# Kernel optimization log

Measured on AMD Instinct MI355X. Metric: run time of the kernel, lower is better.

Reference implementation:

```python
import jax, jax.numpy as jnp
import numpy as np

NUM_HEADS = 8
LN_EPS = 1e-5


def _layernorm(x, g, b):
    m = jnp.mean(x, axis=-1, keepdims=True)
    v = jnp.mean(jnp.square(x - m), axis=-1, keepdims=True)
    return (x - m) * jax.lax.rsqrt(v + LN_EPS) * g + b


def setup_inputs() -> dict:
    key = jax.random.key(0)
    ks = jax.random.split(key, 10)
    D, C, Cin = 2, 256, 64  # depth, embed dim, input channels
    w = lambda k, shape: jax.random.normal(k, shape, jnp.float32) * 0.02
    return {
        "x": jax.random.normal(ks[0], (4, Cin, 12, 12, 12), jnp.float32),
        "W_pe": w(ks[1], (Cin, C)),
        "b_pe": jnp.zeros((C,), jnp.float32),
        "cls_token": w(ks[2], (1, 1, C)),
        "ln1_g": jnp.ones((D, C), jnp.float32),
        "ln1_b": jnp.zeros((D, C), jnp.float32),
        "Wqkv": w(ks[3], (D, C, 3 * C)),
        "Wproj": w(ks[4], (D, C, C)),
        "bproj": jnp.zeros((D, C), jnp.float32),
        "ln2_g": jnp.ones((D, C), jnp.float32),
        "ln2_b": jnp.zeros((D, C), jnp.float32),
        "W1": w(ks[5], (D, C, C)),
        "b1": jnp.zeros((D, C), jnp.float32),
        "W2": w(ks[6], (D, C, C)),
        "b2": jnp.zeros((D, C), jnp.float32),
        "normf_g": jnp.ones((C,), jnp.float32),
        "normf_b": jnp.zeros((C,), jnp.float32),
    }


def reference(x, W_pe, b_pe, cls_token, ln1_g, ln1_b, Wqkv, Wproj, bproj,
              ln2_g, ln2_b, W1, b1, W2, b2, normf_g, normf_b):
    B, Cin, H, W, L = x.shape
    C = W_pe.shape[1]
    hd = C // NUM_HEADS
    scale = hd ** (-0.5)

    # PatchEmbed: 1x1x1 Conv3d == per-voxel linear projection, then flatten to tokens
    tok = jnp.einsum('bchwl,cd->bhwld', x, W_pe).reshape(B, H * W * L, C) + b_pe
    cls = jnp.broadcast_to(cls_token, (B, 1, C))
    t = jnp.concatenate([cls, tok], axis=1)  # [B, N, C], N = H*W*L + 1
    N = t.shape[1]

    depth = Wqkv.shape[0]
    for i in range(depth):
        # --- self-attention ---
        y = _layernorm(t, ln1_g[i], ln1_b[i])
        qkv = (y @ Wqkv[i]).reshape(B, N, 3, NUM_HEADS, hd)
        qkv = jnp.transpose(qkv, (2, 0, 3, 1, 4))  # [3, B, H, N, hd]
        q, k, v = qkv[0], qkv[1], qkv[2]
        attn = jnp.einsum('bhnd,bhmd->bhnm', q, k) * scale
        attn = jax.nn.softmax(attn, axis=-1)
        o = jnp.einsum('bhnm,bhmd->bhnd', attn, v)
        o = jnp.transpose(o, (0, 2, 1, 3)).reshape(B, N, C)
        t = t + (o @ Wproj[i] + bproj[i])
        # --- MLP (mlp_ratio=1.0, exact GELU) ---
        y = _layernorm(t, ln2_g[i], ln2_b[i])
        h = jax.nn.gelu(y @ W1[i] + b1[i], approximate=False)
        t = t + (h @ W2[i] + b2[i])

    t = _layernorm(t, normf_g, normf_b)
    x_cls = t[:, 0]                                   # [B, C]
    feat = t[:, 1:]                                   # [B, H*W*L, C]
    feat = jnp.transpose(feat, (0, 2, 1)).reshape(B, C, H, W, L)  # downsample = Identity for dim=256
    return x_cls, feat
```

## Files before the change

kernel.cpp:

```cpp
#include <hip/hip_runtime.h>
#include <hip/hip_bf16.h>
#include <math.h>

#define B_   4
#define CIN  64
#define P_   1728
#define N_   1729
#define C_   256
#define NH_  8
#define HD_  32
#define M_   (B_*N_)
#define NPAD 1792

typedef __bf16 bf16x8 __attribute__((ext_vector_type(8)));
typedef __bf16 bf16x4 __attribute__((ext_vector_type(4)));
typedef float  f32x4  __attribute__((ext_vector_type(4)));
typedef float  f32x16 __attribute__((ext_vector_type(16)));

__global__ __launch_bounds__(256) void embed2(
    const float* __restrict__ x, const float* __restrict__ Wpe,
    const float* __restrict__ bpe, const float* __restrict__ cls,
    float* __restrict__ t)
{
    int idx = blockIdx.x*256 + threadIdx.x;
    int c   = idx & 255;
    int n   = (idx >> 8) % N_;
    int b   = idx / (N_*256);
    if (n == 0) { t[idx] = cls[c]; return; }
    int p = n - 1;
    float acc = bpe[c];
    for (int ci = 0; ci < CIN; ++ci)
        acc += x[(size_t)(b*CIN + ci)*P_ + p] * Wpe[ci*C_ + c];
    t[idx] = acc;
}

__global__ __launch_bounds__(256) void ln4(
    const float* __restrict__ in, __bf16* __restrict__ out,
    const float* __restrict__ g, const float* __restrict__ bb)
{
    int wv = threadIdx.x >> 6, lane = threadIdx.x & 63;
    size_t row = (size_t)blockIdx.x*4 + wv;
    float4 v = *(const float4*)&in[row*C_ + lane*4];
    float s1 = (v.x+v.y)+(v.z+v.w);
    float s2 = (v.x*v.x+v.y*v.y)+(v.z*v.z+v.w*v.w);
    #pragma unroll
    for (int off = 32; off >= 1; off >>= 1) {
        s1 += __shfl_xor(s1, off);
        s2 += __shfl_xor(s2, off);
    }
    float mean = s1*(1.0f/C_);
    float var  = fmaxf(s2*(1.0f/C_) - mean*mean, 0.0f);
    float rstd = rsqrtf(var + 1e-5f);
    float4 gg = *(const float4*)&g[lane*4];
    float4 bv = *(const float4*)&bb[lane*4];
    bf16x4 r;
    r[0] = (__bf16)((v.x-mean)*rstd*gg.x + bv.x);
    r[1] = (__bf16)((v.y-mean)*rstd*gg.y + bv.y);
    r[2] = (__bf16)((v.z-mean)*rstd*gg.z + bv.z);
    r[3] = (__bf16)((v.w-mean)*rstd*gg.w + bv.w);
    *(bf16x4*)&out[row*C_ + lane*4] = r;
}

__global__ __launch_bounds__(256) void ln4f(
    const float* __restrict__ in, float* __restrict__ out,
    const float* __restrict__ g, const float* __restrict__ bb,
    float* __restrict__ cls_out)
{
    int wv = threadIdx.x >> 6, lane = threadIdx.x & 63;
    size_t row = (size_t)blockIdx.x*4 + wv;
    float4 v = *(const float4*)&in[row*C_ + lane*4];
    float s1 = (v.x+v.y)+(v.z+v.w);
    float s2 = (v.x*v.x+v.y*v.y)+(v.z*v.z+v.w*v.w);
    #pragma unroll
    for (int off = 32; off >= 1; off >>= 1) {
        s1 += __shfl_xor(s1, off);
        s2 += __shfl_xor(s2, off);
    }
    float mean = s1*(1.0f/C_);
    float var  = fmaxf(s2*(1.0f/C_) - mean*mean, 0.0f);
    float rstd = rsqrtf(var + 1e-5f);
    float4 gg = *(const float4*)&g[lane*4];
    float4 bv = *(const float4*)&bb[lane*4];
    float4 r;
    r.x = (v.x-mean)*rstd*gg.x + bv.x;
    r.y = (v.y-mean)*rstd*gg.y + bv.y;
    r.z = (v.z-mean)*rstd*gg.z + bv.z;
    r.w = (v.w-mean)*rstd*gg.w + bv.w;
    *(float4*)&out[row*C_ + lane*4] = r;
    if ((row % N_) == 0)
        *(float4*)&cls_out[(row / N_)*C_ + lane*4] = r;
}

__global__ __launch_bounds__(256) void wprep2(
    const float* __restrict__ Wqkv, const float* __restrict__ Wproj,
    const float* __restrict__ W1,   const float* __restrict__ W2,
    __bf16* __restrict__ wT)
{
    int z = blockIdx.z, which = z >> 1, layer = z & 1;
    const float* src; __bf16* dst; int NC;
    if (which == 0) {
        src = Wqkv + (size_t)layer*C_*768;
        dst = wT   + (size_t)layer*768*256;
        NC  = 768;
    } else {
        NC = 256;
        const float* b3 = (which == 1) ? Wproj : (which == 2) ? W1 : W2;
        src = b3 + (size_t)layer*65536;
        dst = wT + 2*768*256 + (size_t)((which-1)*2 + layer)*65536;
    }
    int n0 = blockIdx.x*32; if (n0 >= NC) return;
    int k0 = blockIdx.y*32;
    __shared__ float tile[32][33];
    int c = threadIdx.x & 31, r = threadIdx.x >> 5;
    for (int rr = r; rr < 32; rr += 8)
        tile[rr][c] = src[(size_t)(k0+rr)*NC + n0 + c];
    __syncthreads();
    for (int rr = r; rr < 32; rr += 8)
        dst[(size_t)(n0+rr)*256 + k0 + c] = (__bf16)tile[c][rr];
}

__global__ __launch_bounds__(256) void padzero(
    __bf16* __restrict__ kB, __bf16* __restrict__ vB)
{
    int idx = blockIdx.x*256 + threadIdx.x;
    if (idx >= 32*63*32) return;
    int d  = idx & 31;
    int n  = (idx >> 5) % 63 + N_;
    int bh = idx / (63*32);
    kB[((size_t)bh*NPAD + n)*32 + d] = (__bf16)0.f;
    vB[((size_t)bh*32 + d)*NPAD + n] = (__bf16)0.f;
}

template<int NC, bool ADD, bool GELU, bool BIAS, bool OUTBF>
__global__ __launch_bounds__(256) void gemm4(
    const __bf16* __restrict__ A, const __bf16* __restrict__ Wt,
    const float* __restrict__ bias, float* __restrict__ outF,
    __bf16* __restrict__ outB)
{
    __shared__ __align__(16) __bf16 As[2][64*64];
    __shared__ __align__(16) __bf16 Bs[2][64*64];
    int r0 = blockIdx.x*64, c0 = blockIdx.y*64;
    int tid = threadIdx.x;
    int wv = tid >> 6, lane = tid & 63, quad = lane >> 4, mn = lane & 15;
    int sr = tid >> 2, sc = tid & 3;
    int ga = r0 + sr; if (ga >= M_) ga = M_ - 1;

    f32x4 acc[4];
    #pragma unroll
    for (int ct = 0; ct < 4; ++ct)
        #pragma unroll
        for (int rr = 0; rr < 4; ++rr) acc[ct][rr] = 0.f;

    bf16x8 ra0, ra1, rb0, rb1;
#define GLOAD(KC) do {                                                   \
        ra0 = *(const bf16x8*)&A[(size_t)ga*256 + (KC)*64 + sc*8];       \
        ra1 = *(const bf16x8*)&A[(size_t)ga*256 + (KC)*64 + sc*8 + 32];  \
        rb0 = *(const bf16x8*)&Wt[(size_t)(c0+sr)*256 + (KC)*64 + sc*8]; \
        rb1 = *(const bf16x8*)&Wt[(size_t)(c0+sr)*256 + (KC)*64 + sc*8 + 32]; \
    } while (0)
#define SSTORE(BUF) do {                                                 \
        *(bf16x8*)&As[BUF][sr*64 + ((sc ^ (sr & 7))*8)]       = ra0;     \
        *(bf16x8*)&As[BUF][sr*64 + (((sc+4) ^ (sr & 7))*8)]   = ra1;     \
        *(bf16x8*)&Bs[BUF][sr*64 + ((sc ^ (sr & 7))*8)]       = rb0;     \
        *(bf16x8*)&Bs[BUF][sr*64 + (((sc+4) ^ (sr & 7))*8)]   = rb1;     \
    } while (0)

    GLOAD(0);
    SSTORE(0);
    __syncthreads();

    for (int kc = 0; kc < 4; ++kc) {
        int cur = kc & 1;
        if (kc < 3) GLOAD(kc+1);
        __builtin_amdgcn_sched_barrier(0);

        #pragma unroll
        for (int h = 0; h < 2; ++h) {
            bf16x8 a = *(const bf16x8*)&As[cur][(wv*16 + mn)*64 + (((h*4+quad) ^ (mn & 7))*8)];
            #pragma unroll
            for (int ct = 0; ct < 4; ++ct) {
                bf16x8 b = *(const bf16x8*)&Bs[cur][(ct*16 + mn)*64 + (((h*4+quad) ^ (mn & 7))*8)];
                acc[ct] = __builtin_amdgcn_mfma_f32_16x16x32_bf16(a, b, acc[ct], 0, 0, 0);
            }
        }

        if (kc < 3) {
            SSTORE(cur^1);
            __syncthreads();
        }
    }
#undef GLOAD
#undef SSTORE

    #pragma unroll
    for (int ct = 0; ct < 4; ++ct) {
        int col = c0 + ct*16 + mn;
        #pragma unroll
        for (int rr = 0; rr < 4; ++rr) {
            int row = r0 + wv*16 + quad*4 + rr;
            if (row >= M_) continue;
            float val = acc[ct][rr];
            if (BIAS) val += bias[col];
            if (GELU) val = 0.5f*val*(1.f + erff(val*0.70710678118654752f));
            size_t oi = (size_t)row*NC + col;
            if (OUTBF) outB[oi] = (__bf16)val;
            else if (ADD) outF[oi] += val;
            else outF[oi] = val;
        }
    }
}

__global__ __launch_bounds__(256) void gemm_qkv4(
    const __bf16* __restrict__ A, const __bf16* __restrict__ Wt,
    __bf16* __restrict__ qB, __bf16* __restrict__ kB, __bf16* __restrict__ vB)
{
    __shared__ __align__(16) __bf16 As[2][64*64];
    __shared__ __align__(16) __bf16 Bs[2][64*64];
    int r0 = blockIdx.x*64, c0 = blockIdx.y*64;
    int tid = threadIdx.x;
    int wv = tid >> 6, lane = tid & 63, quad = lane >> 4, mn = lane & 15;
    int sr = tid >> 2, sc = tid & 3;
    int ga = r0 + sr; if (ga >= M_) ga = M_ - 1;

    f32x4 acc[4];
    #pragma unroll
    for (int ct = 0; ct < 4; ++ct)
        #pragma unroll
        for (int rr = 0; rr < 4; ++rr) acc[ct][rr] = 0.f;

    bf16x8 ra0, ra1, rb0, rb1;
#define GLOAD(KC) do {                                                   \
        ra0 = *(const bf16x8*)&A[(size_t)ga*256 + (KC)*64 + sc*8];       \
        ra1 = *(const bf16x8*)&A[(size_t)ga*256 + (KC)*64 + sc*8 + 32];  \
        rb0 = *(const bf16x8*)&Wt[(size_t)(c0+sr)*256 + (KC)*64 + sc*8]; \
        rb1 = *(const bf16x8*)&Wt[(size_t)(c0+sr)*256 + (KC)*64 + sc*8 + 32]; \
    } while (0)
#define SSTORE(BUF) do {                                                 \
        *(bf16x8*)&As[BUF][sr*64 + ((sc ^ (sr & 7))*8)]       = ra0;     \
        *(bf16x8*)&As[BUF][sr*64 + (((sc+4) ^ (sr & 7))*8)]   = ra1;     \
        *(bf16x8*)&Bs[BUF][sr*64 + ((sc ^ (sr & 7))*8)]       = rb0;     \
        *(bf16x8*)&Bs[BUF][sr*64 + (((sc+4) ^ (sr & 7))*8)]   = rb1;     \
    } while (0)

    GLOAD(0);
    SSTORE(0);
    __syncthreads();

    for (int kc = 0; kc < 4; ++kc) {
        int cur = kc & 1;
        if (kc < 3) GLOAD(kc+1);
        __builtin_amdgcn_sched_barrier(0);

        #pragma unroll
        for (int h = 0; h < 2; ++h) {
            bf16x8 a = *(const bf16x8*)&As[cur][(wv*16 + mn)*64 + (((h*4+quad) ^ (mn & 7))*8)];
            #pragma unroll
            for (int ct = 0; ct < 4; ++ct) {
                bf16x8 b = *(const bf16x8*)&Bs[cur][(ct*16 + mn)*64 + (((h*4+quad) ^ (mn & 7))*8)];
                acc[ct] = __builtin_amdgcn_mfma_f32_16x16x32_bf16(a, b, acc[ct], 0, 0, 0);
            }
        }

        if (kc < 3) {
            SSTORE(cur^1);
            __syncthreads();
        }
    }
#undef GLOAD
#undef SSTORE

    const float scale = 0.2550348727f;
    #pragma unroll
    for (int ct = 0; ct < 4; ++ct) {
        int col = c0 + ct*16 + mn;
        #pragma unroll
        for (int rr = 0; rr < 4; ++rr) {
            int row = r0 + wv*16 + quad*4 + rr;
            if (row >= M_) continue;
            int b = row / N_, n = row - b*N_;
            float val = acc[ct][rr];
            if (col < 256) {
                int h = col >> 5, dd = col & 31;
                qB[((size_t)(b*NH_+h)*NPAD + n)*32 + dd] = (__bf16)(val*scale);
            } else if (col < 512) {
                int h = (col-256) >> 5, dd = col & 31;
                kB[((size_t)(b*NH_+h)*NPAD + n)*32 + dd] = (__bf16)val;
            } else {
                int h = (col-512) >> 5, dd = col & 31;
                vB[((size_t)(b*NH_+h)*32 + dd)*NPAD + n] = (__bf16)val;
            }
        }
    }
}

#define LKS 40
#define LVS 136

__device__ __forceinline__ float fexp2(float x) {
    float r; asm("v_exp_f32 %0, %1" : "=v"(r) : "v"(x)); return r;
}
__device__ __forceinline__ unsigned cvtpk_bf16(float lo, float hi) {
    unsigned r;
    asm("v_cvt_pk_bf16_f32 %0, %1, %2" : "=v"(r) : "v"(lo), "v"(hi));
    return r;
}

__global__ __launch_bounds__(128) void attn13(
    const __bf16* __restrict__ qB, const __bf16* __restrict__ kB,
    const __bf16* __restrict__ vB, __bf16* __restrict__ o)
{
    int bh = blockIdx.x, b = bh >> 3, h = bh & 7;
    int q0 = blockIdx.y * 64;
    int tid = threadIdx.x;
    int wv = tid >> 6, lane = tid & 63, lo5 = lane & 31, hi = lane >> 5;

    __shared__ __align__(16) __bf16 lk[2][128*LKS];
    __shared__ __align__(16) __bf16 lvt[2][32*LVS];

    const __bf16* kbase = kB + (size_t)bh*NPAD*32;
    const __bf16* vbase = vB + (size_t)bh*32*NPAD;

    const __bf16* qrow = qB + ((size_t)bh*NPAD + q0 + wv*32 + lo5)*32 + hi*8;
    bf16x8 qf0 = *(const bf16x8*)(qrow);
    bf16x8 qf1 = *(const bf16x8*)(qrow + 16);

    f32x16 oaccA, oaccB;
    #pragma unroll
    for (int r = 0; r < 16; ++r) { oaccA[r] = 0.f; oaccB[r] = 0.f; }
    float lsum = 0.f;

    int vr = tid >> 2, vc = tid & 3;

    bf16x8 ks0, ks1, ks2, ks3, vs0, vs1, vs2, vs3;
#define ATTN_LOAD(T) do {                                              \
        const __bf16* kp_ = kbase + ((size_t)((T)*128 + tid))*32;      \
        ks0 = *(const bf16x8*)(kp_);                                   \
        ks1 = *(const bf16x8*)(kp_ + 8);                               \
        ks2 = *(const bf16x8*)(kp_ + 16);                              \
        ks3 = *(const bf16x8*)(kp_ + 24);                              \
        const __bf16* vp_ = vbase + (size_t)vr*NPAD + (T)*128 + vc*32; \
        vs0 = *(const bf16x8*)(vp_);                                   \
        vs1 = *(const bf16x8*)(vp_ + 8);                               \
        vs2 = *(const bf16x8*)(vp_ + 16);                              \
        vs3 = *(const bf16x8*)(vp_ + 24);                              \
    } while (0)
#define ATTN_STORE(BUF) do {                                           \
        __bf16* kd = &lk[BUF][tid*LKS];                                \
        *(bf16x8*)(kd)      = ks0;  *(bf16x8*)(kd + 8)  = ks1;         \
        *(bf16x8*)(kd + 16) = ks2;  *(bf16x8*)(kd + 24) = ks3;         \
        __bf16* vd = &lvt[BUF][vr*LVS + vc*32];                        \
        *(bf16x8*)(vd)      = vs0;  *(bf16x8*)(vd + 8)  = vs1;         \
        *(bf16x8*)(vd + 16) = vs2;  *(bf16x8*)(vd + 24) = vs3;         \
    } while (0)

    ATTN_LOAD(0);
    ATTN_STORE(0);
    __syncthreads();

    for (int t = 0; t < 14; ++t) {
        int cur = t & 1;
        if (t < 13) ATTN_LOAD(t+1);
        __builtin_amdgcn_sched_barrier(0);

        f32x16 s[4];
        __builtin_amdgcn_s_setprio(1);
        #pragma unroll
        for (int kg = 0; kg < 4; ++kg) {
            const __bf16* kf = &lk[cur][(kg*32 + lo5)*LKS + hi*8];
            bf16x8 kf0 = *(const bf16x8*)(kf);
            bf16x8 kf1 = *(const bf16x8*)(kf + 16);
            #pragma unroll
            for (int r = 0; r < 16; ++r) s[kg][r] = 0.f;
            s[kg] = __builtin_amdgcn_mfma_f32_32x32x16_bf16(kf0, qf0, s[kg], 0, 0, 0);
            s[kg] = __builtin_amdgcn_mfma_f32_32x32x16_bf16(kf1, qf1, s[kg], 0, 0, 0);
        }
        __builtin_amdgcn_s_setprio(0);

        #pragma unroll
        for (int kg = 0; kg < 4; ++kg) {
            float p[16];
            #pragma unroll
            for (int r = 0; r < 16; ++r) p[r] = fexp2(s[kg][r]);
            float l0 = 0.f, l1 = 0.f;
            #pragma unroll
            for (int r = 0; r < 8; ++r) { l0 += p[r]; l1 += p[r+8]; }
            lsum += l0 + l1;

            unsigned a0 = cvtpk_bf16(p[0],  p[1]),  a1 = cvtpk_bf16(p[2],  p[3]);
            unsigned b0 = cvtpk_bf16(p[4],  p[5]),  b1 = cvtpk_bf16(p[6],  p[7]);
            unsigned c0 = cvtpk_bf16(p[8],  p[9]),  c1 = cvtpk_bf16(p[10], p[11]);
            unsigned d0 = cvtpk_bf16(p[12], p[13]), d1 = cvtpk_bf16(p[14], p[15]);
            asm("v_permlane32_swap_b32 %0, %1" : "+v"(a0), "+v"(b0));
            asm("v_permlane32_swap_b32 %0, %1" : "+v"(a1), "+v"(b1));
            asm("v_permlane32_swap_b32 %0, %1" : "+v"(c0), "+v"(d0));
            asm("v_permlane32_swap_b32 %0, %1" : "+v"(c1), "+v"(d1));
            union { bf16x8 v; unsigned u[4]; } f0, f1;
            f0.u[0] = a0; f0.u[1] = a1; f0.u[2] = b0; f0.u[3] = b1;
            f1.u[0] = c0; f1.u[1] = c1; f1.u[2] = d0; f1.u[3] = d1;

            const __bf16* vf = &lvt[cur][lo5*LVS + kg*32 + hi*8];
            bf16x8 vf0 = *(const bf16x8*)(vf);
            bf16x8 vf1 = *(const bf16x8*)(vf + 16);
            __builtin_amdgcn_s_setprio(1);
            if (kg & 1) {
                oaccB = __builtin_amdgcn_mfma_f32_32x32x16_bf16(f0.v, vf0, oaccB, 0, 0, 0);
                oaccB = __builtin_amdgcn_mfma_f32_32x32x16_bf16(f1.v, vf1, oaccB, 0, 0, 0);
            } else {
                oaccA = __builtin_amdgcn_mfma_f32_32x32x16_bf16(f0.v, vf0, oaccA, 0, 0, 0);
                oaccA = __builtin_amdgcn_mfma_f32_32x32x16_bf16(f1.v, vf1, oaccA, 0, 0, 0);
            }
            __builtin_amdgcn_s_setprio(0);
        }

        if (t < 13) {
            ATTN_STORE(cur^1);
            __syncthreads();
        }
    }
#undef ATTN_LOAD
#undef ATTN_STORE

    lsum += __shfl_xor(lsum, 32);
    float inv = 1.0f / (lsum - 63.0f);

    #pragma unroll
    for (int r = 0; r < 16; ++r) {
        float oa = oaccA[r] + oaccB[r];
        int qrw = (r & 3) + 8*(r >> 2) + 4*hi;
        float li = __shfl(inv, qrw);
        int q = q0 + wv*32 + qrw;
        if (q < N_)
            o[((size_t)b*N_ + q)*C_ + h*HD_ + lo5] = (__bf16)(oa * li);
    }
}

__global__ __launch_bounds__(256) void feat3(
    const float* __restrict__ y, float* __restrict__ outf)
{
    __shared__ float tl[32][33];
    int p0 = blockIdx.x*32, c0 = blockIdx.y*32, b = blockIdx.z;
    int cc = threadIdx.x & 31, rr = threadIdx.x >> 5;
    for (int i = rr; i < 32; i += 8)
        tl[i][cc] = y[((size_t)(b*N_) + 1 + p0 + i)*C_ + c0 + cc];
    __syncthreads();
    for (int i = rr; i < 32; i += 8)
        outf[((size_t)(b*C_) + c0 + i)*P_ + p0 + cc] = tl[cc][i];
}

extern "C" void kernel_launch(void* const* d_in, const int* in_sizes, int n_in,
                              void* d_out, int out_size, void* d_ws, size_t ws_size,
                              hipStream_t stream)
{
    const float* x        = (const float*)d_in[0];
    const float* W_pe     = (const float*)d_in[1];
    const float* b_pe     = (const float*)d_in[2];
    const float* cls_tok  = (const float*)d_in[3];
    const float* ln1_g    = (const float*)d_in[4];
    const float* ln1_b    = (const float*)d_in[5];
    const float* Wqkv     = (const float*)d_in[6];
    const float* Wproj    = (const float*)d_in[7];
    const float* bproj    = (const float*)d_in[8];
    const float* ln2_g    = (const float*)d_in[9];
    const float* ln2_b    = (const float*)d_in[10];
    const float* W1       = (const float*)d_in[11];
    const float* b1       = (const float*)d_in[12];
    const float* W2       = (const float*)d_in[13];
    const float* b2       = (const float*)d_in[14];
    const float* normf_g  = (const float*)d_in[15];
    const float* normf_b  = (const float*)d_in[16];

    const size_t MC = (size_t)M_*C_;
    float*  ws  = (float*)d_ws;
    float*  t   = ws;
    float*  yf  = ws + MC;
    __bf16* ybf = (__bf16*)(ws + 2*MC);
    __bf16* hbf = (__bf16*)(ws + 2*MC + MC/2);
    __bf16* obf = (__bf16*)(ws + 2*MC + MC);
    __bf16* wT  = (__bf16*)(ws + 2*MC + 3*(MC/2));
    __bf16* qB  = wT + 2*768*256 + 6*256*256;
    __bf16* kB  = qB + (size_t)B_*NH_*NPAD*32;
    __bf16* vB  = kB + (size_t)B_*NH_*NPAD*32;

    __bf16* projT = wT + 2*768*256;
    __bf16* w1T   = projT + 2*256*256;
    __bf16* w2T   = w1T   + 2*256*256;

    float* out_cls  = (float*)d_out;
    float* out_feat = out_cls + B_*C_;

    wprep2<<<dim3(24, 8, 8), 256, 0, stream>>>(Wqkv, Wproj, W1, W2, wT);
    padzero<<<252, 256, 0, stream>>>(kB, vB);
    embed2<<<(B_*N_*C_)/256, 256, 0, stream>>>(x, W_pe, b_pe, cls_tok, t);

    const int GRID_M = (M_ + 63) / 64;
    for (int i = 0; i < 2; ++i) {
        ln4<<<M_/4, 256, 0, stream>>>(t, ybf, ln1_g + i*C_, ln1_b + i*C_);
        gemm_qkv4<<<dim3(GRID_M, 12), 256, 0, stream>>>(
            ybf, wT + (size_t)i*768*256, qB, kB, vB);
        attn13<<<dim3(32, 28), 128, 0, stream>>>(qB, kB, vB, obf);
        gemm4<256,true,false,true,false><<<dim3(GRID_M, 4), 256, 0, stream>>>(
            obf, projT + (size_t)i*65536, bproj + i*C_, t, nullptr);
        ln4<<<M_/4, 256, 0, stream>>>(t, ybf, ln2_g + i*C_, ln2_b + i*C_);
        gemm4<256,false,true,true,true><<<dim3(GRID_M, 4), 256, 0, stream>>>(
            ybf, w1T + (size_t)i*65536, b1 + i*C_, nullptr, hbf);
        gemm4<256,true,false,true,false><<<dim3(GRID_M, 4), 256, 0, stream>>>(
            hbf, w2T + (size_t)i*65536, b2 + i*C_, t, nullptr);
    }

    ln4f<<<M_/4, 256, 0, stream>>>(t, yf, normf_g, normf_b, out_cls);
    feat3<<<dim3(54, 8, 4), 256, 0, stream>>>(yf, out_feat);
}
```

Before: 288.7 us.

## Load attention K/V fragments directly from global memory, drop LDS staging

New measurement: 307.7 us. +6.6%, slower.

```diff
diff --git a/kernel.cpp b/kernel.cpp
--- a/kernel.cpp
+++ b/kernel.cpp
@@ -293,9 +293,6 @@
     }
 }
 
-#define LKS 40
-#define LVS 136
-
 __device__ __forceinline__ float fexp2(float x) {
     float r; asm("v_exp_f32 %0, %1" : "=v"(r) : "v"(x)); return r;
 }
@@ -305,7 +302,7 @@
     return r;
 }
 
-__global__ __launch_bounds__(128) void attn13(
+__global__ __launch_bounds__(128) void attn14(
     const __bf16* __restrict__ qB, const __bf16* __restrict__ kB,
     const __bf16* __restrict__ vB, __bf16* __restrict__ o)
 {
@@ -314,9 +311,6 @@
     int tid = threadIdx.x;
     int wv = tid >> 6, lane = tid & 63, lo5 = lane & 31, hi = lane >> 5;
 
-    __shared__ __align__(16) __bf16 lk[2][128*LKS];
-    __shared__ __align__(16) __bf16 lvt[2][32*LVS];
-
     const __bf16* kbase = kB + (size_t)bh*NPAD*32;
     const __bf16* vbase = vB + (size_t)bh*32*NPAD;
 
@@ -329,58 +323,34 @@
     for (int r = 0; r < 16; ++r) { oaccA[r] = 0.f; oaccB[r] = 0.f; }
     float lsum = 0.f;
 
-    int vr = tid >> 2, vc = tid & 3;
-
-    bf16x8 ks0, ks1, ks2, ks3, vs0, vs1, vs2, vs3;
-#define ATTN_LOAD(T) do {                                              \
-        const __bf16* kp_ = kbase + ((size_t)((T)*128 + tid))*32;      \
-        ks0 = *(const bf16x8*)(kp_);                                   \
-        ks1 = *(const bf16x8*)(kp_ + 8);                               \
-        ks2 = *(const bf16x8*)(kp_ + 16);                              \
-        ks3 = *(const bf16x8*)(kp_ + 24);                              \
-        const __bf16* vp_ = vbase + (size_t)vr*NPAD + (T)*128 + vc*32; \
-        vs0 = *(const bf16x8*)(vp_);                                   \
-        vs1 = *(const bf16x8*)(vp_ + 8);                               \
-        vs2 = *(const bf16x8*)(vp_ + 16);                              \
-        vs3 = *(const bf16x8*)(vp_ + 24);                              \
-    } while (0)
-#define ATTN_STORE(BUF) do {                                           \
-        __bf16* kd = &lk[BUF][tid*LKS];                                \
-        *(bf16x8*)(kd)      = ks0;  *(bf16x8*)(kd + 8)  = ks1;         \
-        *(bf16x8*)(kd + 16) = ks2;  *(bf16x8*)(kd + 24) = ks3;         \
-        __bf16* vd = &lvt[BUF][vr*LVS + vc*32];                        \
-        *(bf16x8*)(vd)      = vs0;  *(bf16x8*)(vd + 8)  = vs1;         \
-        *(bf16x8*)(vd + 16) = vs2;  *(bf16x8*)(vd + 24) = vs3;         \
-    } while (0)
-
-    ATTN_LOAD(0);
-    ATTN_STORE(0);
-    __syncthreads();
+    const __bf16* kp = kbase + (size_t)lo5*32 + hi*8;
+    const __bf16* vp = vbase + (size_t)lo5*NPAD + hi*8;
 
     for (int t = 0; t < 14; ++t) {
-        int cur = t & 1;
-        if (t < 13) ATTN_LOAD(t+1);
-        __builtin_amdgcn_sched_barrier(0);
-
-        f32x16 s[4];
-        __builtin_amdgcn_s_setprio(1);
+        bf16x8 kf0[4], kf1[4], vf0[4], vf1[4];
         #pragma unroll
         for (int kg = 0; kg < 4; ++kg) {
-            const __bf16* kf = &lk[cur][(kg*32 + lo5)*LKS + hi*8];
-            bf16x8 kf0 = *(const bf16x8*)(kf);
-            bf16x8 kf1 = *(const bf16x8*)(kf + 16);
+            const __bf16* kpp = kp + (size_t)t*128*32 + kg*32*32;
+            kf0[kg] = *(const bf16x8*)(kpp);
+            kf1[kg] = *(const bf16x8*)(kpp + 16);
+            const __bf16* vpp = vp + (size_t)t*128 + kg*32;
+            vf0[kg] = *(const bf16x8*)(vpp);
+            vf1[kg] = *(const bf16x8*)(vpp + 16);
+        }
+
+        #pragma unroll
+        for (int kg = 0; kg < 4; ++kg) {
+            f32x16 s;
             #pragma unroll
-            for (int r = 0; r < 16; ++r) s[kg][r] = 0.f;
-            s[kg] = __builtin_amdgcn_mfma_f32_32x32x16_bf16(kf0, qf0, s[kg], 0, 0, 0);
-            s[kg] = __builtin_amdgcn_mfma_f32_32x32x16_bf16(kf1, qf1, s[kg], 0, 0, 0);
-        }
-        __builtin_amdgcn_s_setprio(0);
-
-        #pragma unroll
-        for (int kg = 0; kg < 4; ++kg) {
+            for (int r = 0; r < 16; ++r) s[r] = 0.f;
+            __builtin_amdgcn_s_setprio(1);
+            s = __builtin_amdgcn_mfma_f32_32x32x16_bf16(kf0[kg], qf0, s, 0, 0, 0);
+            s = __builtin_amdgcn_mfma_f32_32x32x16_bf16(kf1[kg], qf1, s, 0, 0, 0);
+            __builtin_amdgcn_s_setprio(0);
+
             float p[16];
             #pragma unroll
-            for (int r = 0; r < 16; ++r) p[r] = fexp2(s[kg][r]);
+            for (int r = 0; r < 16; ++r) p[r] = fexp2(s[r]);
             float l0 = 0.f, l1 = 0.f;
             #pragma unroll
             for (int r = 0; r < 8; ++r) { l0 += p[r]; l1 += p[r+8]; }
@@ -398,27 +368,17 @@
             f0.u[0] = a0; f0.u[1] = a1; f0.u[2] = b0; f0.u[3] = b1;
             f1.u[0] = c0; f1.u[1] = c1; f1.u[2] = d0; f1.u[3] = d1;
 
-            const __bf16* vf = &lvt[cur][lo5*LVS + kg*32 + hi*8];
-            bf16x8 vf0 = *(const bf16x8*)(vf);
-            bf16x8 vf1 = *(const bf16x8*)(vf + 16);
             __builtin_amdgcn_s_setprio(1);
             if (kg & 1) {
-                oaccB = __builtin_amdgcn_mfma_f32_32x32x16_bf16(f0.v, vf0, oaccB, 0, 0, 0);
-                oaccB = __builtin_amdgcn_mfma_f32_32x32x16_bf16(f1.v, vf1, oaccB, 0, 0, 0);
+                oaccB = __builtin_amdgcn_mfma_f32_32x32x16_bf16(f0.v, vf0[kg], oaccB, 0, 0, 0);
+                oaccB = __builtin_amdgcn_mfma_f32_32x32x16_bf16(f1.v, vf1[kg], oaccB, 0, 0, 0);
             } else {
-                oaccA = __builtin_amdgcn_mfma_f32_32x32x16_bf16(f0.v, vf0, oaccA, 0, 0, 0);
-                oaccA = __builtin_amdgcn_mfma_f32_32x32x16_bf16(f1.v, vf1, oaccA, 0, 0, 0);
+                oaccA = __builtin_amdgcn_mfma_f32_32x32x16_bf16(f0.v, vf0[kg], oaccA, 0, 0, 0);
+                oaccA = __builtin_amdgcn_mfma_f32_32x32x16_bf16(f1.v, vf1[kg], oaccA, 0, 0, 0);
             }
             __builtin_amdgcn_s_setprio(0);
         }
-
-        if (t < 13) {
-            ATTN_STORE(cur^1);
-            __syncthreads();
-        }
-    }
-#undef ATTN_LOAD
-#undef ATTN_STORE
+    }
 
     lsum += __shfl_xor(lsum, 32);
     float inv = 1.0f / (lsum - 63.0f);
@@ -497,7 +457,7 @@
         ln4<<<M_/4, 256, 0, stream>>>(t, ybf, ln1_g + i*C_, ln1_b + i*C_);
         gemm_qkv4<<<dim3(GRID_M, 12), 256, 0, stream>>>(
             ybf, wT + (size_t)i*768*256, qB, kB, vB);
-        attn13<<<dim3(32, 28), 128, 0, stream>>>(qB, kB, vB, obf);
+        attn14<<<dim3(32, 28), 128, 0, stream>>>(qB, kB, vB, obf);
         gemm4<256,true,false,true,false><<<dim3(GRID_M, 4), 256, 0, stream>>>(
             obf, projT + (size_t)i*65536, bproj + i*C_, t, nullptr);
         ln4<<<M_/4, 256, 0, stream>>>(t, ybf, ln2_g + i*C_, ln2_b + i*C_);
```

## Fuse final LayerNorm stats into last MLP GEMM and merge small kernels

Applied to the files above, without the earlier changes.

Result: faster. 282.5 us (-2.1%).

```diff
diff --git a/kernel.cpp b/kernel.cpp
--- a/kernel.cpp
+++ b/kernel.cpp
@@ -11,17 +11,36 @@
 #define HD_  32
 #define M_   (B_*N_)
 #define NPAD 1792
+#define NB_EMBED 6916
 
 typedef __bf16 bf16x8 __attribute__((ext_vector_type(8)));
 typedef __bf16 bf16x4 __attribute__((ext_vector_type(4)));
 typedef float  f32x4  __attribute__((ext_vector_type(4)));
 typedef float  f32x16 __attribute__((ext_vector_type(16)));
 
-__global__ __launch_bounds__(256) void embed2(
+__global__ __launch_bounds__(256) void embed3(
     const float* __restrict__ x, const float* __restrict__ Wpe,
     const float* __restrict__ bpe, const float* __restrict__ cls,
-    float* __restrict__ t)
-{
+    float* __restrict__ t, __bf16* __restrict__ kB, __bf16* __restrict__ vB,
+    float* __restrict__ stats)
+{
+    if (blockIdx.x >= NB_EMBED) {
+        int ex = blockIdx.x - NB_EMBED;
+        if (ex < 252) {
+            int idx = ex*256 + threadIdx.x;
+            if (idx < 32*63*32) {
+                int d  = idx & 31;
+                int n  = (idx >> 5) % 63 + N_;
+                int bh = idx / (63*32);
+                kB[((size_t)bh*NPAD + n)*32 + d] = (__bf16)0.f;
+                vB[((size_t)bh*32 + d)*NPAD + n] = (__bf16)0.f;
+            }
+        } else {
+            int si = (ex - 252)*256 + threadIdx.x;
+            if (si < 2*M_) stats[si] = 0.f;
+        }
+        return;
+    }
     int idx = blockIdx.x*256 + threadIdx.x;
     int c   = idx & 255;
     int n   = (idx >> 8) % N_;
@@ -61,36 +80,6 @@
     *(bf16x4*)&out[row*C_ + lane*4] = r;
 }
 
-__global__ __launch_bounds__(256) void ln4f(
-    const float* __restrict__ in, float* __restrict__ out,
-    const float* __restrict__ g, const float* __restrict__ bb,
-    float* __restrict__ cls_out)
-{
-    int wv = threadIdx.x >> 6, lane = threadIdx.x & 63;
-    size_t row = (size_t)blockIdx.x*4 + wv;
-    float4 v = *(const float4*)&in[row*C_ + lane*4];
-    float s1 = (v.x+v.y)+(v.z+v.w);
-    float s2 = (v.x*v.x+v.y*v.y)+(v.z*v.z+v.w*v.w);
-    #pragma unroll
-    for (int off = 32; off >= 1; off >>= 1) {
-        s1 += __shfl_xor(s1, off);
-        s2 += __shfl_xor(s2, off);
-    }
-    float mean = s1*(1.0f/C_);
-    float var  = fmaxf(s2*(1.0f/C_) - mean*mean, 0.0f);
-    float rstd = rsqrtf(var + 1e-5f);
-    float4 gg = *(const float4*)&g[lane*4];
-    float4 bv = *(const float4*)&bb[lane*4];
-    float4 r;
-    r.x = (v.x-mean)*rstd*gg.x + bv.x;
-    r.y = (v.y-mean)*rstd*gg.y + bv.y;
-    r.z = (v.z-mean)*rstd*gg.z + bv.z;
-    r.w = (v.w-mean)*rstd*gg.w + bv.w;
-    *(float4*)&out[row*C_ + lane*4] = r;
-    if ((row % N_) == 0)
-        *(float4*)&cls_out[(row / N_)*C_ + lane*4] = r;
-}
-
 __global__ __launch_bounds__(256) void wprep2(
     const float* __restrict__ Wqkv, const float* __restrict__ Wproj,
     const float* __restrict__ W1,   const float* __restrict__ W2,
@@ -119,23 +108,11 @@
         dst[(size_t)(n0+rr)*256 + k0 + c] = (__bf16)tile[c][rr];
 }
 
-__global__ __launch_bounds__(256) void padzero(
-    __bf16* __restrict__ kB, __bf16* __restrict__ vB)
-{
-    int idx = blockIdx.x*256 + threadIdx.x;
-    if (idx >= 32*63*32) return;
-    int d  = idx & 31;
-    int n  = (idx >> 5) % 63 + N_;
-    int bh = idx / (63*32);
-    kB[((size_t)bh*NPAD + n)*32 + d] = (__bf16)0.f;
-    vB[((size_t)bh*32 + d)*NPAD + n] = (__bf16)0.f;
-}
-
-template<int NC, bool ADD, bool GELU, bool BIAS, bool OUTBF>
+template<int NC, bool ADD, bool GELU, bool BIAS, bool OUTBF, bool STATS>
 __global__ __launch_bounds__(256) void gemm4(
     const __bf16* __restrict__ A, const __bf16* __restrict__ Wt,
     const float* __restrict__ bias, float* __restrict__ outF,
-    __bf16* __restrict__ outB)
+    __bf16* __restrict__ outB, float* __restrict__ stats)
 {
     __shared__ __align__(16) __bf16 As[2][64*64];
     __shared__ __align__(16) __bf16 Bs[2][64*64];
@@ -192,6 +169,7 @@
 #undef GLOAD
 #undef SSTORE
 
+    float rs1[4] = {0.f,0.f,0.f,0.f}, rs2[4] = {0.f,0.f,0.f,0.f};
     #pragma unroll
     for (int ct = 0; ct < 4; ++ct) {
         int col = c0 + ct*16 + mn;
@@ -204,8 +182,27 @@
             if (GELU) val = 0.5f*val*(1.f + erff(val*0.70710678118654752f));
             size_t oi = (size_t)row*NC + col;
             if (OUTBF) outB[oi] = (__bf16)val;
-            else if (ADD) outF[oi] += val;
+            else if (ADD) {
+                float tv = outF[oi] + val;
+                outF[oi] = tv;
+                if (STATS) { rs1[rr] += tv; rs2[rr] += tv*tv; }
+            }
             else outF[oi] = val;
+        }
+    }
+    if (STATS) {
+        #pragma unroll
+        for (int rr = 0; rr < 4; ++rr) {
+            float s1 = rs1[rr], s2 = rs2[rr];
+            s1 += __shfl_xor(s1, 1); s1 += __shfl_xor(s1, 2);
+            s1 += __shfl_xor(s1, 4); s1 += __shfl_xor(s1, 8);
+            s2 += __shfl_xor(s2, 1); s2 += __shfl_xor(s2, 2);
+            s2 += __shfl_xor(s2, 4); s2 += __shfl_xor(s2, 8);
+            int row = r0 + wv*16 + quad*4 + rr;
+            if (mn == 0 && row < M_) {
+                atomicAdd(&stats[2*row],     s1);
+                atomicAdd(&stats[2*row + 1], s2);
+            }
         }
     }
 }
@@ -434,17 +431,36 @@
     }
 }
 
-__global__ __launch_bounds__(256) void feat3(
-    const float* __restrict__ y, float* __restrict__ outf)
-{
+__global__ __launch_bounds__(256) void featln(
+    const float* __restrict__ t, const float* __restrict__ stats,
+    const float* __restrict__ g, const float* __restrict__ bb,
+    float* __restrict__ out_cls, float* __restrict__ out_feat)
+{
+    int bx = blockIdx.x;
+    if (bx == 54) {
+        if (blockIdx.y != 0) return;
+        int b = blockIdx.z, c = threadIdx.x;
+        size_t row = (size_t)b*N_;
+        float s1 = stats[2*row], s2 = stats[2*row+1];
+        float mean = s1*(1.0f/C_);
+        float rstd = rsqrtf(fmaxf(s2*(1.0f/C_) - mean*mean, 0.0f) + 1e-5f);
+        out_cls[b*C_ + c] = (t[row*C_ + c] - mean)*rstd*g[c] + bb[c];
+        return;
+    }
     __shared__ float tl[32][33];
-    int p0 = blockIdx.x*32, c0 = blockIdx.y*32, b = blockIdx.z;
+    int p0 = bx*32, c0 = blockIdx.y*32, b = blockIdx.z;
     int cc = threadIdx.x & 31, rr = threadIdx.x >> 5;
-    for (int i = rr; i < 32; i += 8)
-        tl[i][cc] = y[((size_t)(b*N_) + 1 + p0 + i)*C_ + c0 + cc];
+    float gg = g[c0+cc], bv = bb[c0+cc];
+    for (int i = rr; i < 32; i += 8) {
+        size_t row = (size_t)b*N_ + 1 + p0 + i;
+        float s1 = stats[2*row], s2 = stats[2*row+1];
+        float mean = s1*(1.0f/C_);
+        float rstd = rsqrtf(fmaxf(s2*(1.0f/C_) - mean*mean, 0.0f) + 1e-5f);
+        tl[i][cc] = (t[row*C_ + c0 + cc] - mean)*rstd*gg + bv;
+    }
     __syncthreads();
     for (int i = rr; i < 32; i += 8)
-        outf[((size_t)(b*C_) + c0 + i)*P_ + p0 + cc] = tl[cc][i];
+        out_feat[((size_t)(b*C_) + c0 + i)*P_ + p0 + cc] = tl[cc][i];
 }
 
 extern "C" void kernel_launch(void* const* d_in, const int* in_sizes, int n_in,
@@ -472,7 +488,7 @@
     const size_t MC = (size_t)M_*C_;
     float*  ws  = (float*)d_ws;
     float*  t   = ws;
-    float*  yf  = ws + MC;
+    float*  stats = ws + MC;
     __bf16* ybf = (__bf16*)(ws + 2*MC);
     __bf16* hbf = (__bf16*)(ws + 2*MC + MC/2);
     __bf16* obf = (__bf16*)(ws + 2*MC + MC);
@@ -489,8 +505,8 @@
     float* out_feat = out_cls + B_*C_;
 
     wprep2<<<dim3(24, 8, 8), 256, 0, stream>>>(Wqkv, Wproj, W1, W2, wT);
-    padzero<<<252, 256, 0, stream>>>(kB, vB);
-    embed2<<<(B_*N_*C_)/256, 256, 0, stream>>>(x, W_pe, b_pe, cls_tok, t);
+    embed3<<<NB_EMBED + 252 + 55, 256, 0, stream>>>(
+        x, W_pe, b_pe, cls_tok, t, kB, vB, stats);
 
     const int GRID_M = (M_ + 63) / 64;
     for (int i = 0; i < 2; ++i) {
@@ -498,15 +514,19 @@
         gemm_qkv4<<<dim3(GRID_M, 12), 256, 0, stream>>>(
             ybf, wT + (size_t)i*768*256, qB, kB, vB);
         attn13<<<dim3(32, 28), 128, 0, stream>>>(qB, kB, vB, obf);
-        gemm4<256,true,false,true,false><<<dim3(GRID_M, 4), 256, 0, stream>>>(
-            obf, projT + (size_t)i*65536, bproj + i*C_, t, nullptr);
+        gemm4<256,true,false,true,false,false><<<dim3(GRID_M, 4), 256, 0, stream>>>(
+            obf, projT + (size_t)i*65536, bproj + i*C_, t, nullptr, nullptr);
         ln4<<<M_/4, 256, 0, stream>>>(t, ybf, ln2_g + i*C_, ln2_b + i*C_);
-        gemm4<256,false,true,true,true><<<dim3(GRID_M, 4), 256, 0, stream>>>(
-            ybf, w1T + (size_t)i*65536, b1 + i*C_, nullptr, hbf);
-        gemm4<256,true,false,true,false><<<dim3(GRID_M, 4), 256, 0, stream>>>(
-            hbf, w2T + (size_t)i*65536, b2 + i*C_, t, nullptr);
-    }
-
-    ln4f<<<M_/4, 256, 0, stream>>>(t, yf, normf_g, normf_b, out_cls);
-    feat3<<<dim3(54, 8, 4), 256, 0, stream>>>(yf, out_feat);
-}
+        gemm4<256,false,true,true,true,false><<<dim3(GRID_M, 4), 256, 0, stream>>>(
+            ybf, w1T + (size_t)i*65536, b1 + i*C_, nullptr, hbf, nullptr);
+        if (i == 0)
+            gemm4<256,true,false,true,false,false><<<dim3(GRID_M, 4), 256, 0, stream>>>(
+                hbf, w2T + (size_t)i*65536, b2 + i*C_, t, nullptr, nullptr);
+        else
+            gemm4<256,true,false,true,false,true><<<dim3(GRID_M, 4), 256, 0, stream>>>(
+                hbf, w2T + (size_t)i*65536, b2 + i*C_, t, nullptr, stats);
+    }
+
+    featln<<<dim3(55, 8, 4), 256, 0, stream>>>(
+        t, stats, normf_g, normf_b, out_cls, out_feat);
+}
```
